# Performance work log

Hardware: AMD Instinct MI355X
Metric: run time of the kernel (lower is better)

The kernel has to match this reference:

```python
import jax, jax.numpy as jnp
import numpy as np

DIM = 1024
HEADS = 16
HDIM = DIM // HEADS
MLP_HID = 4096
LN_EPS = 1e-5
NORM_EPS = 1e-12  # F.normalize eps


def _layernorm(x, g, b):
    mu = jnp.mean(x, axis=-1, keepdims=True)
    var = jnp.mean(jnp.square(x - mu), axis=-1, keepdims=True)
    return (x - mu) / jnp.sqrt(var + LN_EPS) * g + b


def _l2norm(x):
    n = jnp.linalg.norm(x, axis=-1, keepdims=True)
    return x / jnp.maximum(n, NORM_EPS)


def setup_inputs() -> dict:
    key = jax.random.key(0)
    ks = jax.random.split(key, 8)
    s = 0.02
    x = jax.random.normal(ks[0], (2, 2048, DIM), dtype=jnp.float32)
    w_qkv = jax.random.normal(ks[1], (3 * DIM, DIM), dtype=jnp.float32) * s  # torch Linear weight (out,in)
    w_proj = jax.random.normal(ks[2], (DIM, DIM), dtype=jnp.float32) * s
    temp = jnp.ones((HEADS, 1, 1), dtype=jnp.float32)
    w1 = jax.random.normal(ks[3], (MLP_HID, DIM), dtype=jnp.float32) * s
    b1 = jnp.zeros((MLP_HID,), dtype=jnp.float32)
    w2 = jax.random.normal(ks[4], (DIM, MLP_HID), dtype=jnp.float32) * s
    b2 = jnp.zeros((DIM,), dtype=jnp.float32)
    ln1_g = jnp.ones((DIM,), dtype=jnp.float32)
    ln1_b = jnp.zeros((DIM,), dtype=jnp.float32)
    ln2_g = jnp.ones((DIM,), dtype=jnp.float32)
    ln2_b = jnp.zeros((DIM,), dtype=jnp.float32)
    return {"x": x, "ln1_g": ln1_g, "ln1_b": ln1_b, "w_qkv": w_qkv,
            "w_proj": w_proj, "temp": temp, "ln2_g": ln2_g, "ln2_b": ln2_b,
            "w1": w1, "b1": b1, "w2": w2, "b2": b2}


def reference(x, ln1_g, ln1_b, w_qkv, w_proj, temp, ln2_g, ln2_b, w1, b1, w2, b2):
    b, n, c = x.shape
    # --- MHSA with L2-normalized q,k and learnable per-head temperature ---
    h = _layernorm(x, ln1_g, ln1_b)
    qkv = h @ w_qkv.T                             # [b,n,3c]
    qkv = qkv.reshape(b, n, 3, HEADS, HDIM).transpose(2, 0, 3, 1, 4)  # [3,b,h,n,d]
    q, k, v = qkv[0], qkv[1], qkv[2]
    q = _l2norm(q)
    k = _l2norm(k)
    attn = jnp.einsum('bhnd,bhmd->bhnm', q, k) * temp  # temp [h,1,1] broadcasts
    attn = jax.nn.softmax(attn, axis=-1)
    out = jnp.einsum('bhnm,bhmd->bhnd', attn, v)       # [b,h,n,d]
    out = out.transpose(0, 2, 1, 3).reshape(b, n, c)
    x = x + out @ w_proj.T
    # --- MLP ---
    h = _layernorm(x, ln2_g, ln2_b)
    h = jax.nn.gelu(h @ w1.T + b1, approximate=False)
    x = x + h @ w2.T + b2
    return x
```

## Files before the change

### kernel.cpp

```cpp
#include <hip/hip_runtime.h>
#include <cstdint>
#include <cstddef>

typedef unsigned short u16;
typedef __attribute__((ext_vector_type(8))) short short8;
typedef __attribute__((ext_vector_type(4))) float f32x4;
typedef __attribute__((ext_vector_type(4))) float float4v;
typedef __attribute__((ext_vector_type(4))) u16 u16x4;

__device__ __forceinline__ u16 f2bf(float f) {
  union { float f; uint32_t u; } v; v.f = f;
  uint32_t u = v.u;
  return (u16)((u + 0x7FFFu + ((u >> 16) & 1u)) >> 16);
}
__device__ __forceinline__ float bf2f(u16 s) {
  union { uint32_t u; float f; } v; v.u = ((uint32_t)s) << 16; return v.f;
}

__device__ __forceinline__ float fast_exp2(float x) {
#if __has_builtin(__builtin_amdgcn_exp2f)
  return __builtin_amdgcn_exp2f(x);
#else
  return exp2f(x);
#endif
}

__device__ __forceinline__ void gload16(const u16* g, u16* l) {
  __builtin_amdgcn_global_load_lds((const __attribute__((address_space(1))) void*)g,
                                   (__attribute__((address_space(3))) void*)l,
                                   16, 0, 0);
}

#define SBAR __builtin_amdgcn_sched_barrier(0)

__global__ __launch_bounds__(256) void k_cvt(const float* __restrict__ in, u16* __restrict__ out, int n4) {
  int i = blockIdx.x * 256 + threadIdx.x;
  if (i >= n4) return;
  float4v v = *(const float4v*)(in + (size_t)i * 4);
  u16x4 o;
  #pragma unroll
  for (int j = 0; j < 4; j++) o[j] = f2bf(v[j]);
  *(u16x4*)(out + (size_t)i * 4) = o;
}

__global__ __launch_bounds__(256) void k_ln(const float* __restrict__ x, const float* __restrict__ g,
                                            const float* __restrict__ b, u16* __restrict__ out) {
  int row = blockIdx.x, tid = threadIdx.x;
  int wid = tid >> 6;
  const float* xr = x + (size_t)row * 1024;
  float4v v = *(const float4v*)(xr + tid * 4);
  float s = v[0] + v[1] + v[2] + v[3];
  float sq = v[0]*v[0] + v[1]*v[1] + v[2]*v[2] + v[3]*v[3];
  #pragma unroll
  for (int m = 1; m <= 32; m <<= 1) { s += __shfl_xor(s, m); sq += __shfl_xor(sq, m); }
  __shared__ float ss[4], ssq[4];
  if ((tid & 63) == 0) { ss[wid] = s; ssq[wid] = sq; }
  __syncthreads();
  s = ss[0] + ss[1] + ss[2] + ss[3];
  sq = ssq[0] + ssq[1] + ssq[2] + ssq[3];
  float mu = s * (1.0f/1024.0f);
  float var = sq * (1.0f/1024.0f) - mu*mu;
  float rs = rsqrtf(var + 1e-5f);
  u16x4 o;
  #pragma unroll
  for (int j = 0; j < 4; j++) {
    float y = (v[j] - mu) * rs * g[tid*4+j] + b[tid*4+j];
    o[j] = f2bf(y);
  }
  *(u16x4*)(out + (size_t)row * 1024 + tid * 4) = o;
}

__global__ __launch_bounds__(256) void k_redln(const float* __restrict__ x, const u16* __restrict__ P,
                                               const float* __restrict__ g, const float* __restrict__ b,
                                               float* __restrict__ x1, u16* __restrict__ h2) {
  int row = blockIdx.x, tid = threadIdx.x;
  int wid = tid >> 6;
  size_t off = (size_t)row * 1024 + tid * 4;
  float4v v = *(const float4v*)(x + off);
  #pragma unroll
  for (int z = 0; z < 4; z++) {
    u16x4 p = *(const u16x4*)(P + (size_t)z * 4194304 + off);
    #pragma unroll
    for (int j = 0; j < 4; j++) v[j] += bf2f(p[j]);
  }
  *(float4v*)(x1 + off) = v;
  float s = v[0] + v[1] + v[2] + v[3];
  float sq = v[0]*v[0] + v[1]*v[1] + v[2]*v[2] + v[3]*v[3];
  #pragma unroll
  for (int m = 1; m <= 32; m <<= 1) { s += __shfl_xor(s, m); sq += __shfl_xor(sq, m); }
  __shared__ float ss[4], ssq[4];
  if ((tid & 63) == 0) { ss[wid] = s; ssq[wid] = sq; }
  __syncthreads();
  s = ss[0] + ss[1] + ss[2] + ss[3];
  sq = ssq[0] + ssq[1] + ssq[2] + ssq[3];
  float mu = s * (1.0f/1024.0f);
  float var = sq * (1.0f/1024.0f) - mu*mu;
  float rs = rsqrtf(var + 1e-5f);
  u16x4 o;
  #pragma unroll
  for (int j = 0; j < 4; j++) o[j] = f2bf((v[j] - mu) * rs * g[tid*4+j] + b[tid*4+j]);
  *(u16x4*)(h2 + off) = o;
}

template<int EPI>
__global__ __launch_bounds__(512, 2) void k_g256(const u16* __restrict__ A, const u16* __restrict__ B,
                                                 const float* __restrict__ bias, u16* __restrict__ Cb,
                                                 int M, int N, int K, int Ksub) {
  extern __shared__ __align__(16) u16 smem[];
  int tid = threadIdx.x;
  int gx = gridDim.x;
  int lin = blockIdx.y * gx + blockIdx.x;
  int nwg = gx * gridDim.y;
  int cpx = nwg >> 3;
  int swz = (lin & 7) * cpx + (lin >> 3);
  int bx = swz % gx, by = swz / gx;
  int m0 = by * 256, n0 = bx * 256;
  int kbase = blockIdx.z * Ksub;
  int wid = tid >> 6, lane = tid & 63;
  int wm = wid >> 2, wn = wid & 3;
  int l15 = lane & 15, l16 = lane >> 4;

  f32x4 acc[8][4] = {};
  int nt = Ksub >> 6;

  auto STAGE = [&](int bsel, int kb) {
    #pragma unroll
    for (int st = 0; st < 2; st++) {
      u16* abase = smem + bsel*32768 + st*16384;
      u16* bbase = abase + 8192;
      int kbs = kb + st*32;
      #pragma unroll
      for (int i = 0; i < 2; i++) {
        int c = i*512 + tid;
        int R = c >> 3, p = c & 7;
        int sp = p ^ (R & 7);
        int r = 2*R + (sp >> 2);
        int g = sp & 3;
        gload16(A + (size_t)(m0 + r)*K + kbs + g*8, abase + c*8);
        gload16(B + (size_t)(n0 + r)*K + kbs + g*8, bbase + c*8);
      }
    }
  };

  STAGE(0, kbase);

  for (int t = 0; t < nt; ++t) {
    int sl = t & 1;
    asm volatile("s_waitcnt vmcnt(0)" ::: "memory");
    SBAR;
    __builtin_amdgcn_s_barrier();
    SBAR;
    if (t + 1 < nt) STAGE(sl ^ 1, kbase + (t + 1) * 64);
    #pragma unroll
    for (int st = 0; st < 2; st++) {
      const u16* ab = smem + sl*32768 + st*16384;
      const u16* bb = ab + 8192;
      short8 af[8], bf[4];
      #pragma unroll
      for (int mf = 0; mf < 8; mf++) {
        int r = wm*128 + mf*16 + l15;
        int R = r >> 1;
        int sp = ((r & 1)*4 + l16) ^ (R & 7);
        af[mf] = *(const short8*)(ab + R*64 + sp*8);
      }
      #pragma unroll
      for (int nf = 0; nf < 4; nf++) {
        int r = wn*64 + nf*16 + l15;
        int R = r >> 1;
        int sp = ((r & 1)*4 + l16) ^ (R & 7);
        bf[nf] = *(const short8*)(bb + R*64 + sp*8);
      }
      asm volatile("s_waitcnt lgkmcnt(0)" ::: "memory");
      SBAR;
      __builtin_amdgcn_s_setprio(1);
      #pragma unroll
      for (int mf = 0; mf < 8; mf++)
        #pragma unroll
        for (int nf = 0; nf < 4; nf++)
          acc[mf][nf] = __builtin_amdgcn_mfma_f32_16x16x32_bf16(af[mf], bf[nf], acc[mf][nf], 0, 0, 0);
      __builtin_amdgcn_s_setprio(0);
    }
  }

  size_t zoff = (EPI == 6) ? (size_t)blockIdx.z * M * N : 0;
  #pragma unroll
  for (int mf = 0; mf < 8; mf++) {
    #pragma unroll
    for (int nf = 0; nf < 4; nf++) {
      int col = n0 + wn*64 + nf*16 + l15;
      #pragma unroll
      for (int r = 0; r < 4; r++) {
        int row = m0 + wm*128 + mf*16 + l16*4 + r;
        float v = acc[mf][nf][r];
        if constexpr (EPI == 2) { v += bias[col]; v = 0.5f*v*(1.0f + erff(v*0.70710678118f)); }
        Cb[zoff + (size_t)row*N + col] = f2bf(v);
      }
    }
  }
}

template<int HASB>
__global__ __launch_bounds__(256) void k_red4(const float* __restrict__ base, const float* __restrict__ bias,
                                              const u16* __restrict__ P, float* __restrict__ out) {
  int i = blockIdx.x * 256 + threadIdx.x;
  float4v v = *(const float4v*)(base + (size_t)i * 4);
  if constexpr (HASB) {
    float4v bb = *(const float4v*)(bias + (size_t)(i & 255) * 4);
    #pragma unroll
    for (int j = 0; j < 4; j++) v[j] += bb[j];
  }
  #pragma unroll
  for (int z = 0; z < 4; z++) {
    u16x4 p = *(const u16x4*)(P + (size_t)z * 4194304 + (size_t)i * 4);
    #pragma unroll
    for (int j = 0; j < 4; j++) v[j] += bf2f(p[j]);
  }
  *(float4v*)(out + (size_t)i * 4) = v;
}

__global__ __launch_bounds__(256) void k_prep(const u16* __restrict__ qkv, const float* __restrict__ temp,
                                              u16* __restrict__ Qn, u16* __restrict__ Kn, u16* __restrict__ Vt) {
  int grp = blockIdx.x, bh = blockIdx.y;
  int b = bh >> 4, h = bh & 15;
  int tid = threadIdx.x;
  int n0 = grp * 64;
  __shared__ __align__(16) u16 vs[64*64];
  float tmp = temp[h] * 1.44269504f;
  int j8 = tid & 7;
  #pragma unroll
  for (int pass = 0; pass < 2; pass++) {
    int tl = pass*32 + (tid >> 3);
    size_t roff = (size_t)((b*2048) + n0 + tl) * 3072 + h*64 + j8*8;
    short8 q8 = *(const short8*)(qkv + roff);
    short8 k8 = *(const short8*)(qkv + roff + 1024);
    short8 v8 = *(const short8*)(qkv + roff + 2048);
    float qv[8], kv[8];
    float sq = 0.f, sk = 0.f;
    #pragma unroll
    for (int jj = 0; jj < 8; jj++) {
      qv[jj] = bf2f((u16)q8[jj]); sq += qv[jj]*qv[jj];
      kv[jj] = bf2f((u16)k8[jj]); sk += kv[jj]*kv[jj];
    }
    sq += __shfl_xor(sq, 1); sq += __shfl_xor(sq, 2); sq += __shfl_xor(sq, 4);
    sk += __shfl_xor(sk, 1); sk += __shfl_xor(sk, 2); sk += __shfl_xor(sk, 4);
    float qs = tmp / fmaxf(sqrtf(sq), 1e-12f);
    float ksc = 1.0f / fmaxf(sqrtf(sk), 1e-12f);
    short8 qo, ko;
    #pragma unroll
    for (int jj = 0; jj < 8; jj++) {
      qo[jj] = (short)f2bf(qv[jj] * qs);
      ko[jj] = (short)f2bf(kv[jj] * ksc);
    }
    size_t obase = ((size_t)bh*2048 + n0 + tl)*64 + j8*8;
    *(short8*)(Qn + obase) = qo;
    *(short8*)(Kn + obase) = ko;
    *(short8*)&vs[tl*64 + j8*8] = v8;
  }
  __syncthreads();
  int d = tid & 63, chunk = tid >> 6;
  u16 vals[16];
  #pragma unroll
  for (int jj = 0; jj < 16; jj++) vals[jj] = vs[(chunk*16 + jj)*64 + d];
  short8 w0, w1v;
  #pragma unroll
  for (int j = 0; j < 8; j++) { w0[j] = (short)vals[j]; w1v[j] = (short)vals[8+j]; }
  size_t vo = ((size_t)bh*64 + d)*2048 + n0 + chunk*16;
  *(short8*)(Vt + vo) = w0;
  *(short8*)(Vt + vo + 8) = w1v;
}

__device__ __forceinline__ int akey(int row) { return (row & 3) | (((row >> 3) & 1) << 2); }

__global__ __launch_bounds__(256) void k_attn(const u16* __restrict__ Qn, const u16* __restrict__ Kn,
                                              const u16* __restrict__ Vt, const float* __restrict__ temp,
                                              u16* __restrict__ Out) {
  __shared__ __align__(16) u16 Ks[2][64*64];
  __shared__ __align__(16) u16 Vs[2][64*64];
  int lin = blockIdx.y * gridDim.x + blockIdx.x;
  int c = lin & 7, t5 = lin >> 3;
  int bh = c*4 + (t5 >> 4);
  int qg = t5 & 15;
  int b = bh >> 4, h = bh & 15;
  int tid = threadIdx.x, wid = tid >> 6, lane = tid & 63;
  int l15 = lane & 15, l16 = lane >> 4;
  size_t base = (size_t)bh * 2048 * 64;
  size_t vbase = (size_t)bh * 64 * 2048;
  int q0 = qg*128 + wid*32;
  float m2 = fabsf(temp[h]) * 1.44269504f;
  short8 qf[2][2];
  #pragma unroll
  for (int g = 0; g < 2; g++)
    #pragma unroll
    for (int ks = 0; ks < 2; ks++)
      qf[g][ks] = *(const short8*)(Qn + base + (size_t)(q0 + g*16 + l15)*64 + ks*32 + l16*8);
  f32x4 o[2][4] = {};
  float lrow[2] = {0.f, 0.f};
  int prow = (l15 & 3) + 8*(l15 >> 2);

  auto STAGE = [&](int bsel, int kv0) {
    #pragma unroll
    for (int i = 0; i < 2; i++) {
      int cc = i*256 + tid;
      int row = cc >> 3, p = cc & 7;
      int g = p ^ akey(row);
      gload16(Kn + base + (size_t)(kv0 + row)*64 + g*8, &Ks[bsel][(i*256 + wid*64)*8]);
      gload16(Vt + vbase + (size_t)row*2048 + kv0 + g*8, &Vs[bsel][(i*256 + wid*64)*8]);
    }
  };

  STAGE(0, 0);
  __syncthreads();
  int cur = 0;
  for (int kv0 = 0; kv0 < 2048; kv0 += 64) {
    if (kv0 + 64 < 2048) STAGE(cur ^ 1, kv0 + 64);
    f32x4 s[2][4] = {};
    #pragma unroll
    for (int dks = 0; dks < 2; dks++) {
      #pragma unroll
      for (int ss = 0; ss < 4; ss++) {
        int row = (ss & 1)*4 + (ss >> 1)*32 + prow;
        short8 kf = *(const short8*)&Ks[cur][row*64 + ((dks*4 + l16) ^ akey(row))*8];
        s[0][ss] = __builtin_amdgcn_mfma_f32_16x16x32_bf16(kf, qf[0][dks], s[0][ss], 0, 0, 0);
        s[1][ss] = __builtin_amdgcn_mfma_f32_16x16x32_bf16(kf, qf[1][dks], s[1][ss], 0, 0, 0);
      }
    }
    short8 pf[2][2];
    #pragma unroll
    for (int g = 0; g < 2; g++) {
      float tsum = 0.f;
      #pragma unroll
      for (int kvs = 0; kvs < 2; kvs++) {
        float e[8];
        #pragma unroll
        for (int r = 0; r < 4; r++) {
          e[r]   = fast_exp2(s[g][kvs*2][r]   - m2);
          e[4+r] = fast_exp2(s[g][kvs*2+1][r] - m2);
        }
        #pragma unroll
        for (int r = 0; r < 8; r++) tsum += e[r];
        union { uint32_t u[4]; short8 v; } pu;
        #pragma unroll
        for (int w = 0; w < 4; w++) {
          uint32_t pk;
          asm("v_cvt_pk_bf16_f32 %0, %1, %2" : "=v"(pk) : "v"(e[2*w]), "v"(e[2*w+1]));
          pu.u[w] = pk;
        }
        pf[g][kvs] = pu.v;
      }
      lrow[g] += tsum;
    }
    #pragma unroll
    for (int kvs = 0; kvs < 2; kvs++) {
      short8 vf[4];
      #pragma unroll
      for (int dt = 0; dt < 4; dt++) {
        int row = dt*16 + l15;
        vf[dt] = *(const short8*)&Vs[cur][row*64 + (((kvs*4 + l16) ^ akey(row))*8)];
      }
      #pragma unroll
      for (int dt = 0; dt < 4; dt++) {
        o[0][dt] = __builtin_amdgcn_mfma_f32_16x16x32_bf16(vf[dt], pf[0][kvs], o[0][dt], 0, 0, 0);
        o[1][dt] = __builtin_amdgcn_mfma_f32_16x16x32_bf16(vf[dt], pf[1][kvs], o[1][dt], 0, 0, 0);
      }
    }
    __syncthreads();
    cur ^= 1;
  }
  #pragma unroll
  for (int g = 0; g < 2; g++) {
    float l = lrow[g];
    l += __shfl_xor(l, 16);
    l += __shfl_xor(l, 32);
    float rl = 1.0f / l;
    int tok = b*2048 + q0 + g*16 + l15;
    #pragma unroll
    for (int dt = 0; dt < 4; dt++) {
      u16x4 ov;
      #pragma unroll
      for (int r = 0; r < 4; r++) ov[r] = f2bf(o[g][dt][r] * rl);
      *(u16x4*)(Out + (size_t)tok*1024 + h*64 + dt*16 + l16*4) = ov;
    }
  }
}

static constexpr size_t OFF_WQKV  = 0;
static constexpr size_t OFF_WPROJ = OFF_WQKV  + 6291456;
static constexpr size_t OFF_W1    = OFF_WPROJ + 2097152;
static constexpr size_t OFF_W2    = OFF_W1    + 8388608;
static constexpr size_t OFF_HBF   = OFF_W2    + 8388608;
static constexpr size_t OFF_H2BF  = OFF_HBF   + 8388608;
static constexpr size_t OFF_QKVBF = OFF_H2BF  + 8388608;
static constexpr size_t OFF_QN    = OFF_QKVBF + 25165824;
static constexpr size_t OFF_KN    = OFF_QN    + 8388608;
static constexpr size_t OFF_VT    = OFF_KN    + 8388608;
static constexpr size_t OFF_AOUT  = OFF_VT    + 8388608;
static constexpr size_t OFF_X1    = OFF_AOUT  + 8388608;
static constexpr size_t OFF_HID   = OFF_X1    + 16777216;

extern "C" void kernel_launch(void* const* d_in, const int* in_sizes, int n_in,
                              void* d_out, int out_size, void* d_ws, size_t ws_size,
                              hipStream_t stream) {
  (void)in_sizes; (void)n_in; (void)out_size; (void)ws_size;
  const float* x     = (const float*)d_in[0];
  const float* ln1g  = (const float*)d_in[1];
  const float* ln1b  = (const float*)d_in[2];
  const float* wqkv  = (const float*)d_in[3];
  const float* wproj = (const float*)d_in[4];
  const float* temp  = (const float*)d_in[5];
  const float* ln2g  = (const float*)d_in[6];
  const float* ln2b  = (const float*)d_in[7];
  const float* w1    = (const float*)d_in[8];
  const float* b1    = (const float*)d_in[9];
  const float* w2    = (const float*)d_in[10];
  const float* b2    = (const float*)d_in[11];

  char* ws = (char*)d_ws;
  u16* wqkv_bf  = (u16*)(ws + OFF_WQKV);
  u16* wproj_bf = (u16*)(ws + OFF_WPROJ);
  u16* w1_bf    = (u16*)(ws + OFF_W1);
  u16* w2_bf    = (u16*)(ws + OFF_W2);
  u16* h_bf     = (u16*)(ws + OFF_HBF);
  u16* h2_bf    = (u16*)(ws + OFF_H2BF);
  u16* qkv_bf   = (u16*)(ws + OFF_QKVBF);
  u16* Qn       = (u16*)(ws + OFF_QN);
  u16* Kn       = (u16*)(ws + OFF_KN);
  u16* Vt       = (u16*)(ws + OFF_VT);
  u16* aout_bf  = (u16*)(ws + OFF_AOUT);
  float* x1     = (float*)(ws + OFF_X1);
  u16* hid_bf   = (u16*)(ws + OFF_HID);
  u16* part_p   = (u16*)(ws + OFF_HID);
  u16* part_m   = (u16*)(ws + OFF_QN);
  float* outf   = (float*)d_out;

  static bool attr_done = false;
  if (!attr_done) {
    hipFuncSetAttribute((const void*)k_g256<2>, hipFuncAttributeMaxDynamicSharedMemorySize, 131072);
    hipFuncSetAttribute((const void*)k_g256<4>, hipFuncAttributeMaxDynamicSharedMemorySize, 131072);
    hipFuncSetAttribute((const void*)k_g256<6>, hipFuncAttributeMaxDynamicSharedMemorySize, 131072);
    attr_done = true;
  }

  k_cvt<<<3072, 256, 0, stream>>>(wqkv,  wqkv_bf,  786432);
  k_cvt<<<1024, 256, 0, stream>>>(wproj, wproj_bf, 262144);
  k_cvt<<<4096, 256, 0, stream>>>(w1,    w1_bf,    1048576);
  k_cvt<<<4096, 256, 0, stream>>>(w2,    w2_bf,    1048576);

  k_ln<<<4096, 256, 0, stream>>>(x, ln1g, ln1b, h_bf);
  k_g256<4><<<dim3(12, 16), 512, 131072, stream>>>(h_bf, wqkv_bf, nullptr, qkv_bf, 4096, 3072, 1024, 1024);
  k_prep<<<dim3(32, 32), 256, 0, stream>>>(qkv_bf, temp, Qn, Kn, Vt);
  k_attn<<<dim3(16, 32), 256, 0, stream>>>(Qn, Kn, Vt, temp, aout_bf);
  k_g256<6><<<dim3(4, 16, 4), 512, 131072, stream>>>(aout_bf, wproj_bf, nullptr, part_p, 4096, 1024, 1024, 256);
  k_redln<<<4096, 256, 0, stream>>>(x, part_p, ln2g, ln2b, x1, h2_bf);
  k_g256<2><<<dim3(16, 16), 512, 131072, stream>>>(h2_bf, w1_bf, b1, hid_bf, 4096, 4096, 1024, 1024);
  k_g256<6><<<dim3(4, 16, 4), 512, 131072, stream>>>(hid_bf, w2_bf, nullptr, part_m, 4096, 1024, 4096, 1024);
  k_red4<1><<<4096, 256, 0, stream>>>(x1, b2, part_m, outf);
}
```

Baseline: 242.1 us.

## Split-K the MLP up GEMM and deepen split-K on the down GEMM

```diff
diff --git a/kernel.cpp b/kernel.cpp
--- a/kernel.cpp
+++ b/kernel.cpp
@@ -199,9 +199,9 @@
   }
 }
 
-template<int HASB>
-__global__ __launch_bounds__(256) void k_red4(const float* __restrict__ base, const float* __restrict__ bias,
-                                              const u16* __restrict__ P, float* __restrict__ out) {
+template<int NP, int HASB>
+__global__ __launch_bounds__(256) void k_red(const float* __restrict__ base, const float* __restrict__ bias,
+                                             const u16* __restrict__ P, size_t zstride, float* __restrict__ out) {
   int i = blockIdx.x * 256 + threadIdx.x;
   float4v v = *(const float4v*)(base + (size_t)i * 4);
   if constexpr (HASB) {
@@ -210,12 +210,30 @@
     for (int j = 0; j < 4; j++) v[j] += bb[j];
   }
   #pragma unroll
-  for (int z = 0; z < 4; z++) {
-    u16x4 p = *(const u16x4*)(P + (size_t)z * 4194304 + (size_t)i * 4);
+  for (int z = 0; z < NP; z++) {
+    u16x4 p = *(const u16x4*)(P + (size_t)z * zstride + (size_t)i * 4);
     #pragma unroll
     for (int j = 0; j < 4; j++) v[j] += bf2f(p[j]);
   }
   *(float4v*)(out + (size_t)i * 4) = v;
+}
+
+__global__ __launch_bounds__(256) void k_redg(const u16* __restrict__ P, const float* __restrict__ b1,
+                                              u16* __restrict__ hid) {
+  int i = blockIdx.x * 256 + threadIdx.x;
+  size_t off = (size_t)i * 4;
+  int col = (int)(off & 4095);
+  u16x4 p0 = *(const u16x4*)(P + off);
+  u16x4 p1 = *(const u16x4*)(P + 16777216 + off);
+  float4v bb = *(const float4v*)(b1 + col);
+  u16x4 o;
+  #pragma unroll
+  for (int j = 0; j < 4; j++) {
+    float v = bf2f(p0[j]) + bf2f(p1[j]) + bb[j];
+    v = 0.5f*v*(1.0f + erff(v*0.70710678118f));
+    o[j] = f2bf(v);
+  }
+  *(u16x4*)(hid + off) = o;
 }
 
 __global__ __launch_bounds__(256) void k_prep(const u16* __restrict__ qkv, const float* __restrict__ temp,
@@ -388,14 +406,15 @@
 static constexpr size_t OFF_W1    = OFF_WPROJ + 2097152;
 static constexpr size_t OFF_W2    = OFF_W1    + 8388608;
 static constexpr size_t OFF_HBF   = OFF_W2    + 8388608;
-static constexpr size_t OFF_H2BF  = OFF_HBF   + 8388608;
-static constexpr size_t OFF_QKVBF = OFF_H2BF  + 8388608;
+static constexpr size_t OFF_QKVBF = OFF_HBF   + 8388608;
 static constexpr size_t OFF_QN    = OFF_QKVBF + 25165824;
 static constexpr size_t OFF_KN    = OFF_QN    + 8388608;
 static constexpr size_t OFF_VT    = OFF_KN    + 8388608;
 static constexpr size_t OFF_AOUT  = OFF_VT    + 8388608;
-static constexpr size_t OFF_X1    = OFF_AOUT  + 8388608;
+static constexpr size_t OFF_H2BF  = OFF_AOUT  + 8388608;
+static constexpr size_t OFF_X1    = OFF_H2BF  + 8388608;
 static constexpr size_t OFF_HID   = OFF_X1    + 16777216;
+static constexpr size_t OFF_PART  = OFF_HBF;
 
 extern "C" void kernel_launch(void* const* d_in, const int* in_sizes, int n_in,
                               void* d_out, int out_size, void* d_ws, size_t ws_size,
@@ -429,7 +448,7 @@
   float* x1     = (float*)(ws + OFF_X1);
   u16* hid_bf   = (u16*)(ws + OFF_HID);
   u16* part_p   = (u16*)(ws + OFF_HID);
-  u16* part_m   = (u16*)(ws + OFF_QN);
+  u16* part     = (u16*)(ws + OFF_PART);
   float* outf   = (float*)d_out;
 
   static bool attr_done = false;
@@ -451,7 +470,8 @@
   k_attn<<<dim3(16, 32), 256, 0, stream>>>(Qn, Kn, Vt, temp, aout_bf);
   k_g256<6><<<dim3(4, 16, 4), 512, 131072, stream>>>(aout_bf, wproj_bf, nullptr, part_p, 4096, 1024, 1024, 256);
   k_redln<<<4096, 256, 0, stream>>>(x, part_p, ln2g, ln2b, x1, h2_bf);
-  k_g256<2><<<dim3(16, 16), 512, 131072, stream>>>(h2_bf, w1_bf, b1, hid_bf, 4096, 4096, 1024, 1024);
-  k_g256<6><<<dim3(4, 16, 4), 512, 131072, stream>>>(hid_bf, w2_bf, nullptr, part_m, 4096, 1024, 4096, 1024);
-  k_red4<1><<<4096, 256, 0, stream>>>(x1, b2, part_m, outf);
-}
+  k_g256<6><<<dim3(16, 16, 2), 512, 131072, stream>>>(h2_bf, w1_bf, nullptr, part, 4096, 4096, 1024, 512);
+  k_redg<<<16384, 256, 0, stream>>>(part, b1, hid_bf);
+  k_g256<6><<<dim3(4, 16, 8), 512, 131072, stream>>>(hid_bf, w2_bf, nullptr, part, 4096, 1024, 4096, 512);
+  k_red<8,1><<<4096, 256, 0, stream>>>(x1, b2, part, 4194304, outf);
+}
```

Measured after the change: 271.6 us. +12.2%, slower.
